# Kernel optimization log

Hardware: AMD Instinct MI355X
Metric: run time of the kernel (lower is better)

The kernel has to match this reference:

```python
import jax, jax.numpy as jnp
import numpy as np

B, S, DM, H = 4, 2048, 768, 12
HD = DM // H
HEAD_Z = float(np.sqrt(HD))


def norm_layer(x, scale, bias):
    # custom normalization over last dim: (x - mean)/std * scale + bias, scalar scale/bias, no eps
    mean = x.mean(axis=2, keepdims=True)
    std = jnp.sqrt(((x - mean) ** 2).mean(axis=2, keepdims=True))
    return (x - mean) / std * scale + bias


def setup_inputs() -> dict:
    key = jax.random.key(0)
    ks = jax.random.split(key, 12)
    s = 1.0 / np.sqrt(DM)
    return {
        "base": jax.random.normal(ks[0], (B, S, DM), dtype=jnp.float32),
        "Wqkv": jax.random.normal(ks[1], (DM, 3 * DM), dtype=jnp.float32) * s,
        "bqkv": jax.random.normal(ks[2], (3 * DM,), dtype=jnp.float32) * s,
        "W1": jax.random.normal(ks[3], (DM, DM), dtype=jnp.float32) * s,
        "b1": jax.random.normal(ks[4], (DM,), dtype=jnp.float32) * s,
        "W2": jax.random.normal(ks[5], (DM, DM), dtype=jnp.float32) * s,
        "b2": jax.random.normal(ks[6], (DM,), dtype=jnp.float32) * s,
        "n1_scale": jax.random.uniform(ks[7], (1,), jnp.float32, -s, s) + 0.5,
        "n1_bias": jax.random.uniform(ks[8], (1,), jnp.float32, -s, s),
        "n2_scale": jax.random.uniform(ks[9], (1,), jnp.float32, -s, s) + 0.5,
        "n2_bias": jax.random.uniform(ks[10], (1,), jnp.float32, -s, s),
    }


def reference(base, Wqkv, bqkv, W1, b1, W2, b2, n1_scale, n1_bias, n2_scale, n2_bias):
    qkv = base @ Wqkv + bqkv                     # [B,S,3*DM]
    q, k, v = jnp.split(qkv, 3, axis=2)
    # per-head attention, vectorized over heads: the torch loop with broadcast-mul-sum
    # is mathematically softmax(QK^T/sqrt(hd)) @ V per head
    q = q.reshape(B, S, H, HD)
    k = k.reshape(B, S, H, HD)
    v = v.reshape(B, S, H, HD)
    scores = jnp.einsum('bqhd,bkhd->bhqk', q, k) / HEAD_Z  # [B,H,S,S]
    attn = jax.nn.softmax(scores, axis=-1)
    av = jnp.einsum('bhqk,bkhd->bqhd', attn, v).reshape(B, S, DM)
    hidden = norm_layer(av @ W1 + b1 + base, n1_scale, n1_bias)
    out = norm_layer(jax.nn.relu(hidden @ W2 + b2) + hidden, n2_scale, n2_bias)
    return out
```

## Files before the change

### kernel.cpp

```cpp
#include <hip/hip_runtime.h>
#include <hip/hip_bf16.h>
#include <stdint.h>

#define B_ 4
#define S_ 2048
#define DM_ 768
#define H_ 12
#define HD_ 64
#define ROWS (B_*S_)
#define QKVN (3*DM_)

typedef __attribute__((ext_vector_type(8))) short short8;
typedef __attribute__((ext_vector_type(4))) float floatx4;
typedef __attribute__((ext_vector_type(8))) unsigned short ushort8;
typedef __attribute__((ext_vector_type(4))) unsigned short ushort4v;
typedef __attribute__((ext_vector_type(4))) float float4_t;

__device__ __forceinline__ unsigned short f2b(float f) {
  union { float f; uint32_t u; } x; x.f = f;
  uint32_t r = x.u + 0x7FFFu + ((x.u >> 16) & 1u);
  return (unsigned short)(r >> 16);
}
__device__ __forceinline__ float b2f(unsigned short u) {
  union { uint32_t u; float f; } x; x.u = ((uint32_t)u) << 16; return x.f;
}
__device__ __forceinline__ uint32_t fbits(float f) {
  union { float f; uint32_t u; } x; x.f = f; return x.u;
}

__device__ __forceinline__ void load_lds16(const void* g, void* l) {
  __builtin_amdgcn_global_load_lds(
      (const __attribute__((address_space(1))) uint32_t*)g,
      (__attribute__((address_space(3))) uint32_t*)l, 16, 0, 0);
}

#define CVT_B 6144
#define WQ_B 1728
#define W1_B 576
__global__ __launch_bounds__(256) void prep(
    const float* __restrict__ base, unsigned short* __restrict__ base_bf,
    const float* __restrict__ Wqkv, unsigned short* __restrict__ Wqkvt,
    const float* __restrict__ W1, unsigned short* __restrict__ W1t,
    const float* __restrict__ W2, unsigned short* __restrict__ W2t) {
  __shared__ float t[32][33];
  int bid = blockIdx.x;
  int tid = threadIdx.x;
  if (bid < CVT_B) {
    int i = bid * 256 + tid;
    float4_t v = ((const float4_t*)base)[i];
    ushort4v o;
    o[0] = f2b(v[0]); o[1] = f2b(v[1]); o[2] = f2b(v[2]); o[3] = f2b(v[3]);
    ((ushort4v*)base_bf)[i] = o;
    return;
  }
  const float* W; unsigned short* Wt; int N, rel;
  if (bid < CVT_B + WQ_B)      { W = Wqkv; Wt = Wqkvt; N = QKVN; rel = bid - CVT_B; }
  else if (bid < CVT_B + WQ_B + W1_B) { W = W1; Wt = W1t; N = DM_; rel = bid - CVT_B - WQ_B; }
  else                          { W = W2; Wt = W2t; N = DM_; rel = bid - CVT_B - WQ_B - W1_B; }
  int K = DM_;
  int n0 = (rel % (N / 32)) * 32, k0 = (rel / (N / 32)) * 32;
  int tx = tid & 31, ty = tid >> 5;
#pragma unroll
  for (int i = 0; i < 4; i++)
    t[ty + i * 8][tx] = W[(size_t)(k0 + ty + i * 8) * N + n0 + tx];
  __syncthreads();
#pragma unroll
  for (int i = 0; i < 4; i++)
    Wt[(size_t)(n0 + ty + i * 8) * K + k0 + tx] = f2b(t[tx][ty + i * 8]);
}

__global__ __launch_bounds__(256) void vtrans(const unsigned short* __restrict__ qkv,
                                              unsigned short* __restrict__ Vt) {
  int st = blockIdx.x;
  int bh = blockIdx.y;
  int b = bh / H_, h = bh % H_;
  __shared__ unsigned short t[64][65];
  int tid = threadIdx.x;
#pragma unroll
  for (int i = 0; i < 2; i++) {
    int c = i * 256 + tid;
    int r = c >> 3, o = (c & 7) * 8;
    ushort8 v = *(const ushort8*)(qkv + (size_t)(b * S_ + st * 64 + r) * QKVN + 2 * DM_ + h * HD_ + o);
#pragma unroll
    for (int j = 0; j < 8; j++) t[r][o + j] = v[j];
  }
  __syncthreads();
#pragma unroll
  for (int i = 0; i < 2; i++) {
    int c = i * 256 + tid;
    int d = c >> 3, o = (c & 7) * 8;
    ushort8 v;
#pragma unroll
    for (int j = 0; j < 8; j++) {
      int p = o + j;
      int s = ((p & 3) << 4) | (p >> 2);
      v[j] = t[s][d];
    }
    *(ushort8*)(Vt + (size_t)(bh * 64 + d) * S_ + st * 64 + o) = v;
  }
}

__global__ __launch_bounds__(256, 2) void gemm_qkv(
    const unsigned short* __restrict__ A,
    const unsigned short* __restrict__ Bt,
    const float* __restrict__ bias,
    unsigned short* __restrict__ Cout,
    int M, int N, int K) {
  __shared__ __align__(16) unsigned short As[128 * 64];
  __shared__ __align__(16) unsigned short Bs[128 * 64];
  int tid = threadIdx.x;
  int wave = tid >> 6, lane = tid & 63;
  int quad = lane >> 4, l16 = lane & 15;
  int e = l16 & 7;
  int sr = lane >> 3;
  int sc = (lane & 7) ^ (sr & 7);
  int m0 = blockIdx.y * 128, n0 = blockIdx.x * 128;
  int wm = (wave >> 1) * 64, wn = (wave & 1) * 64;
  floatx4 acc[4][4] = {};
  int c0 = wave * 4;

  for (int kb = 0; kb < K; kb += 64) {
#pragma unroll
    for (int i = 0; i < 4; i++) {
      int op = c0 + i;
      load_lds16(A + (size_t)(m0 + op * 8 + sr) * K + kb + sc * 8, (char*)As + op * 1024);
    }
#pragma unroll
    for (int i = 0; i < 4; i++) {
      int op = c0 + i;
      load_lds16(Bt + (size_t)(n0 + op * 8 + sr) * K + kb + sc * 8, (char*)Bs + op * 1024);
    }
    __syncthreads();
#pragma unroll
    for (int ks = 0; ks < 2; ks++) {
      short8 af[4], bfr[4];
#pragma unroll
      for (int mt = 0; mt < 4; mt++)
        af[mt] = *(const short8*)(As + (wm + mt * 16 + l16) * 64 + ((ks * 4 + quad) ^ e) * 8);
#pragma unroll
      for (int nt = 0; nt < 4; nt++)
        bfr[nt] = *(const short8*)(Bs + (wn + nt * 16 + l16) * 64 + ((ks * 4 + quad) ^ e) * 8);
#pragma unroll
      for (int mt = 0; mt < 4; mt++)
#pragma unroll
        for (int nt = 0; nt < 4; nt++)
          acc[mt][nt] = __builtin_amdgcn_mfma_f32_16x16x32_bf16(af[mt], bfr[nt], acc[mt][nt], 0, 0, 0);
    }
    __syncthreads();
  }
#pragma unroll
  for (int mt = 0; mt < 4; mt++) {
#pragma unroll
    for (int nt = 0; nt < 4; nt++) {
#pragma unroll
      for (int r = 0; r < 4; r++) {
        int row = m0 + wm + mt * 16 + quad * 4 + r;
        int col = n0 + wn + nt * 16 + l16;
        size_t idx = (size_t)row * N + col;
        float v = acc[mt][nt][r] + bias[col];
        if (col < DM_) v *= 0.18033688011112042f;
        Cout[idx] = f2b(v);
      }
    }
  }
}

template <int EPI>
__global__ __launch_bounds__(256, 4) void gemm64(
    const unsigned short* __restrict__ A,
    const unsigned short* __restrict__ Bt,
    const float* __restrict__ bias,
    const unsigned short* __restrict__ res,
    unsigned short* __restrict__ Cout,
    int M, int N, int K) {
  __shared__ __align__(16) unsigned short As[64 * 64];
  __shared__ __align__(16) unsigned short Bs[128 * 64];
  int tid = threadIdx.x;
  int wave = tid >> 6, lane = tid & 63;
  int quad = lane >> 4, l16 = lane & 15;
  int e = l16 & 7;
  int sr = lane >> 3;
  int sc = (lane & 7) ^ (sr & 7);
  int m0 = blockIdx.y * 64, n0 = blockIdx.x * 128;
  int wm = (wave >> 1) * 32, wn = (wave & 1) * 64;
  floatx4 acc[2][4] = {};

  for (int kb = 0; kb < K; kb += 64) {
#pragma unroll
    for (int i = 0; i < 2; i++) {
      int op = wave * 2 + i;
      load_lds16(A + (size_t)(m0 + op * 8 + sr) * K + kb + sc * 8, (char*)As + op * 1024);
    }
#pragma unroll
    for (int i = 0; i < 4; i++) {
      int op = wave * 4 + i;
      load_lds16(Bt + (size_t)(n0 + op * 8 + sr) * K + kb + sc * 8, (char*)Bs + op * 1024);
    }
    __syncthreads();
#pragma unroll
    for (int ks = 0; ks < 2; ks++) {
      short8 af[2], bfr[4];
#pragma unroll
      for (int mt = 0; mt < 2; mt++)
        af[mt] = *(const short8*)(As + (wm + mt * 16 + l16) * 64 + ((ks * 4 + quad) ^ e) * 8);
#pragma unroll
      for (int nt = 0; nt < 4; nt++)
        bfr[nt] = *(const short8*)(Bs + (wn + nt * 16 + l16) * 64 + ((ks * 4 + quad) ^ e) * 8);
#pragma unroll
      for (int mt = 0; mt < 2; mt++)
#pragma unroll
        for (int nt = 0; nt < 4; nt++)
          acc[mt][nt] = __builtin_amdgcn_mfma_f32_16x16x32_bf16(af[mt], bfr[nt], acc[mt][nt], 0, 0, 0);
    }
    __syncthreads();
  }
#pragma unroll
  for (int mt = 0; mt < 2; mt++) {
#pragma unroll
    for (int nt = 0; nt < 4; nt++) {
#pragma unroll
      for (int r = 0; r < 4; r++) {
        int row = m0 + wm + mt * 16 + quad * 4 + r;
        int col = n0 + wn + nt * 16 + l16;
        size_t idx = (size_t)row * N + col;
        float v = acc[mt][nt][r] + bias[col];
        if (EPI == 2) v = fmaxf(v, 0.0f);
        v += b2f(res[idx]);
        Cout[idx] = f2b(v);
      }
    }
  }
}

__global__ __launch_bounds__(256, 2) void attn(
    const unsigned short* __restrict__ qkv,
    const unsigned short* __restrict__ Vt,
    unsigned short* __restrict__ av) {
  int qt = blockIdx.x;
  int bh = blockIdx.y;
  int b = bh / H_, h = bh % H_;
  int row0 = b * S_ + qt * 128;
  __shared__ __align__(16) unsigned short Ks[2][64 * 64];
  __shared__ __align__(16) unsigned short Vs[2][64 * 64];
  __shared__ __align__(16) unsigned short Ps[4][32 * 72];
  int tid = threadIdx.x;
  int wave = tid >> 6, lane = tid & 63;
  int quad = lane >> 4, l16 = lane & 15;
  int e = l16 & 7;
  int sr = lane >> 3;
  int sc = (lane & 7) ^ (sr & 7);

#pragma unroll
  for (int i = 0; i < 4; i++) {
    load_lds16(qkv + (size_t)(row0 + wave * 32 + i * 8 + sr) * QKVN + h * HD_ + sc * 8,
               (char*)Ps[wave] + i * 1024);
  }
  const unsigned short* kp = qkv + (size_t)(b * S_ + wave * 16 + sr) * QKVN + DM_ + h * HD_ + sc * 8;
  const unsigned short* vp = Vt + ((size_t)bh * 64 + wave * 16 + sr) * S_ + sc * 8;
  auto stageKV = [&](const unsigned short* kq, const unsigned short* vq, int buf) {
#pragma unroll
    for (int i = 0; i < 2; i++) {
      load_lds16(kq + (size_t)i * 8 * QKVN, (char*)Ks[buf] + wave * 2048 + i * 1024);
      load_lds16(vq + (size_t)i * 8 * S_, (char*)Vs[buf] + wave * 2048 + i * 1024);
    }
  };
  stageKV(kp, vp, 0);

  floatx4 accO[2][4] = {};
  floatx4 accL[2] = {};
  short8 ones;
#pragma unroll
  for (int j = 0; j < 8; j++) ones[j] = (short)0x3F80;
  __syncthreads();

  short8 qf[2][2];
#pragma unroll
  for (int mf = 0; mf < 2; mf++)
#pragma unroll
    for (int ks = 0; ks < 2; ks++)
      qf[mf][ks] = *(const short8*)(Ps[wave] + (mf * 16 + l16) * 64 + ((ks * 4 + quad) ^ e) * 8);

  int cur = 0;
  for (int kt = 0; kt < 32; kt++) {
    floatx4 sv[2][4] = {};
#pragma unroll
    for (int ks = 0; ks < 2; ks++)
#pragma unroll
      for (int nt = 0; nt < 4; nt++) {
        short8 kf = *(const short8*)(Ks[cur] + (nt * 16 + l16) * 64 + ((ks * 4 + quad) ^ e) * 8);
#pragma unroll
        for (int mf = 0; mf < 2; mf++)
          sv[mf][nt] = __builtin_amdgcn_mfma_f32_16x16x32_bf16(qf[mf][ks], kf, sv[mf][nt], 0, 0, 0);
      }
    if (kt + 1 < 32) {
      kp += 64 * QKVN;
      vp += 64;
      stageKV(kp, vp, cur ^ 1);
    }
#pragma unroll
    for (int mf = 0; mf < 2; mf++)
#pragma unroll
      for (int r = 0; r < 4; r++) {
        uint32_t u0 = fbits(__builtin_amdgcn_exp2f(sv[mf][0][r]));
        uint32_t u1 = fbits(__builtin_amdgcn_exp2f(sv[mf][1][r]));
        uint32_t u2 = fbits(__builtin_amdgcn_exp2f(sv[mf][2][r]));
        uint32_t u3 = fbits(__builtin_amdgcn_exp2f(sv[mf][3][r]));
        uint2 val;
        val.x = __builtin_amdgcn_perm(u1, u0, 0x07060302u);
        val.y = __builtin_amdgcn_perm(u3, u2, 0x07060302u);
        *(uint2*)(&Ps[wave][(mf * 16 + quad * 4 + r) * 72 + l16 * 4]) = val;
      }
#pragma unroll
    for (int ks = 0; ks < 2; ks++) {
      short8 pf[2];
#pragma unroll
      for (int mf = 0; mf < 2; mf++) {
        pf[mf] = *(const short8*)(Ps[wave] + (mf * 16 + l16) * 72 + ks * 32 + quad * 8);
        accL[mf] = __builtin_amdgcn_mfma_f32_16x16x32_bf16(pf[mf], ones, accL[mf], 0, 0, 0);
      }
#pragma unroll
      for (int nt = 0; nt < 4; nt++) {
        short8 vf = *(const short8*)(Vs[cur] + (nt * 16 + l16) * 64 + ((ks * 4 + quad) ^ e) * 8);
#pragma unroll
        for (int mf = 0; mf < 2; mf++)
          accO[mf][nt] = __builtin_amdgcn_mfma_f32_16x16x32_bf16(pf[mf], vf, accO[mf][nt], 0, 0, 0);
      }
    }
    __syncthreads();
    cur ^= 1;
  }
#pragma unroll
  for (int mf = 0; mf < 2; mf++)
#pragma unroll
    for (int r = 0; r < 4; r++) {
      float inv = 1.0f / accL[mf][r];
      int row = row0 + wave * 32 + mf * 16 + quad * 4 + r;
#pragma unroll
      for (int nt = 0; nt < 4; nt++)
        av[(size_t)row * DM_ + h * HD_ + nt * 16 + l16] = f2b(accO[mf][nt][r] * inv);
    }
}

template <int WB>
__global__ __launch_bounds__(256) void normk(
    const unsigned short* __restrict__ X, const float* __restrict__ scale,
    const float* __restrict__ bias, float* __restrict__ Y,
    unsigned short* __restrict__ Ybf) {
  int row = blockIdx.x;
  const unsigned short* x = X + (size_t)row * DM_;
  int tid = threadIdx.x;
  int wave = tid >> 6, lane = tid & 63;
  float v[3];
#pragma unroll
  for (int i = 0; i < 3; i++) v[i] = b2f(x[tid + i * 256]);
  float s = v[0] + v[1] + v[2];
#pragma unroll
  for (int o = 32; o > 0; o >>= 1) s += __shfl_xor(s, o);
  __shared__ float red[4];
  if (lane == 0) red[wave] = s;
  __syncthreads();
  float mean = (red[0] + red[1] + red[2] + red[3]) * (1.0f / DM_);
  float ss = 0.0f;
#pragma unroll
  for (int i = 0; i < 3; i++) { v[i] -= mean; ss += v[i] * v[i]; }
#pragma unroll
  for (int o = 32; o > 0; o >>= 1) ss += __shfl_xor(ss, o);
  __syncthreads();
  if (lane == 0) red[wave] = ss;
  __syncthreads();
  float var = (red[0] + red[1] + red[2] + red[3]) * (1.0f / DM_);
  float rstd = rsqrtf(var);
  float sg = scale[0], bg = bias[0];
#pragma unroll
  for (int i = 0; i < 3; i++) {
    float y = v[i] * rstd * sg + bg;
    if (WB) Ybf[(size_t)row * DM_ + tid + i * 256] = f2b(y);
    else    Y[(size_t)row * DM_ + tid + i * 256] = y;
  }
}

extern "C" void kernel_launch(void* const* d_in, const int* in_sizes, int n_in,
                              void* d_out, int out_size, void* d_ws, size_t ws_size,
                              hipStream_t stream) {
  const float* base = (const float*)d_in[0];
  const float* Wqkv = (const float*)d_in[1];
  const float* bqkv = (const float*)d_in[2];
  const float* W1 = (const float*)d_in[3];
  const float* b1 = (const float*)d_in[4];
  const float* W2 = (const float*)d_in[5];
  const float* b2 = (const float*)d_in[6];
  const float* n1s = (const float*)d_in[7];
  const float* n1b = (const float*)d_in[8];
  const float* n2s = (const float*)d_in[9];
  const float* n2b = (const float*)d_in[10];
  float* out = (float*)d_out;

  char* ws = (char*)d_ws;
  size_t off = 0;
  auto alloc = [&](size_t bytes) {
    char* p = ws + off;
    off = (off + bytes + 255) & ~(size_t)255;
    return p;
  };
  unsigned short* base_bf = (unsigned short*)alloc((size_t)ROWS * DM_ * 2);
  unsigned short* Wqkvt = (unsigned short*)alloc((size_t)QKVN * DM_ * 2);
  unsigned short* W1t = (unsigned short*)alloc((size_t)DM_ * DM_ * 2);
  unsigned short* W2t = (unsigned short*)alloc((size_t)DM_ * DM_ * 2);
  unsigned short* qkvb = (unsigned short*)alloc((size_t)ROWS * QKVN * 2);
  unsigned short* Vtb = (unsigned short*)alloc((size_t)B_ * H_ * HD_ * S_ * 2);
  unsigned short* avb = (unsigned short*)alloc((size_t)ROWS * DM_ * 2);
  unsigned short* t1b = (unsigned short*)alloc((size_t)ROWS * DM_ * 2);
  unsigned short* hbf = (unsigned short*)alloc((size_t)ROWS * DM_ * 2);

  prep<<<CVT_B + WQ_B + 2 * W1_B, 256, 0, stream>>>(
      base, base_bf, Wqkv, Wqkvt, W1, W1t, W2, W2t);
  gemm_qkv<<<dim3(QKVN / 128, ROWS / 128), 256, 0, stream>>>(
      base_bf, Wqkvt, bqkv, qkvb, ROWS, QKVN, DM_);
  vtrans<<<dim3(S_ / 64, B_ * H_), 256, 0, stream>>>(qkvb, Vtb);
  attn<<<dim3(S_ / 128, B_ * H_), 256, 0, stream>>>(qkvb, Vtb, avb);
  gemm64<1><<<dim3(DM_ / 128, ROWS / 64), 256, 0, stream>>>(
      avb, W1t, b1, base_bf, t1b, ROWS, DM_, DM_);
  normk<1><<<ROWS, 256, 0, stream>>>(t1b, n1s, n1b, nullptr, hbf);
  gemm64<2><<<dim3(DM_ / 128, ROWS / 64), 256, 0, stream>>>(
      hbf, W2t, b2, hbf, t1b, ROWS, DM_, DM_);
  normk<0><<<ROWS, 256, 0, stream>>>(t1b, n2s, n2b, out, nullptr);
}
```

Before: 258.2 us.

## Fuse V transpose into QKV GEMM epilogue and widen K tile to 128

Removes the separate vtrans kernel. The QKV GEMM now writes the V block directly in transposed per-head layout, staging through LDS in the epilogue, and writes Q and K normally. The K-step is doubled to 128 with a 16-way XOR swizzle, which halves the number of barriers per tile. In exchange, LDS use rises to 64KB per block, which may reduce occupancy below the launch bound's target of 2 blocks. The transposed layout must match what attn expects, since the old vtrans applied a permuted s ordering.

```diff
diff --git a/kernel.cpp b/kernel.cpp
--- a/kernel.cpp
+++ b/kernel.cpp
@@ -69,77 +69,50 @@
     Wt[(size_t)(n0 + ty + i * 8) * K + k0 + tx] = f2b(t[tx][ty + i * 8]);
 }
 
-__global__ __launch_bounds__(256) void vtrans(const unsigned short* __restrict__ qkv,
-                                              unsigned short* __restrict__ Vt) {
-  int st = blockIdx.x;
-  int bh = blockIdx.y;
-  int b = bh / H_, h = bh % H_;
-  __shared__ unsigned short t[64][65];
-  int tid = threadIdx.x;
-#pragma unroll
-  for (int i = 0; i < 2; i++) {
-    int c = i * 256 + tid;
-    int r = c >> 3, o = (c & 7) * 8;
-    ushort8 v = *(const ushort8*)(qkv + (size_t)(b * S_ + st * 64 + r) * QKVN + 2 * DM_ + h * HD_ + o);
-#pragma unroll
-    for (int j = 0; j < 8; j++) t[r][o + j] = v[j];
-  }
-  __syncthreads();
-#pragma unroll
-  for (int i = 0; i < 2; i++) {
-    int c = i * 256 + tid;
-    int d = c >> 3, o = (c & 7) * 8;
-    ushort8 v;
-#pragma unroll
-    for (int j = 0; j < 8; j++) {
-      int p = o + j;
-      int s = ((p & 3) << 4) | (p >> 2);
-      v[j] = t[s][d];
-    }
-    *(ushort8*)(Vt + (size_t)(bh * 64 + d) * S_ + st * 64 + o) = v;
-  }
-}
-
 __global__ __launch_bounds__(256, 2) void gemm_qkv(
     const unsigned short* __restrict__ A,
     const unsigned short* __restrict__ Bt,
     const float* __restrict__ bias,
     unsigned short* __restrict__ Cout,
+    unsigned short* __restrict__ Vt,
     int M, int N, int K) {
-  __shared__ __align__(16) unsigned short As[128 * 64];
-  __shared__ __align__(16) unsigned short Bs[128 * 64];
+  __shared__ __align__(16) unsigned short LDSbuf[2 * 128 * 128];
+  unsigned short* As = LDSbuf;
+  unsigned short* Bs = LDSbuf + 128 * 128;
   int tid = threadIdx.x;
   int wave = tid >> 6, lane = tid & 63;
   int quad = lane >> 4, l16 = lane & 15;
-  int e = l16 & 7;
-  int sr = lane >> 3;
-  int sc = (lane & 7) ^ (sr & 7);
+  int sr4 = lane >> 4;
+  int c16 = lane & 15;
   int m0 = blockIdx.y * 128, n0 = blockIdx.x * 128;
   int wm = (wave >> 1) * 64, wn = (wave & 1) * 64;
   floatx4 acc[4][4] = {};
-  int c0 = wave * 4;
-
-  for (int kb = 0; kb < K; kb += 64) {
-#pragma unroll
-    for (int i = 0; i < 4; i++) {
-      int op = c0 + i;
-      load_lds16(A + (size_t)(m0 + op * 8 + sr) * K + kb + sc * 8, (char*)As + op * 1024);
-    }
-#pragma unroll
-    for (int i = 0; i < 4; i++) {
-      int op = c0 + i;
-      load_lds16(Bt + (size_t)(n0 + op * 8 + sr) * K + kb + sc * 8, (char*)Bs + op * 1024);
+
+  for (int kb = 0; kb < K; kb += 128) {
+#pragma unroll
+    for (int i = 0; i < 8; i++) {
+      int op = wave * 8 + i;
+      int srow = op * 4 + sr4;
+      int sc = c16 ^ (srow & 15);
+      load_lds16(A + (size_t)(m0 + srow) * K + kb + sc * 8, (char*)As + op * 1024);
+    }
+#pragma unroll
+    for (int i = 0; i < 8; i++) {
+      int op = wave * 8 + i;
+      int srow = op * 4 + sr4;
+      int sc = c16 ^ (srow & 15);
+      load_lds16(Bt + (size_t)(n0 + srow) * K + kb + sc * 8, (char*)Bs + op * 1024);
     }
     __syncthreads();
 #pragma unroll
-    for (int ks = 0; ks < 2; ks++) {
+    for (int ks = 0; ks < 4; ks++) {
       short8 af[4], bfr[4];
 #pragma unroll
       for (int mt = 0; mt < 4; mt++)
-        af[mt] = *(const short8*)(As + (wm + mt * 16 + l16) * 64 + ((ks * 4 + quad) ^ e) * 8);
+        af[mt] = *(const short8*)(As + (wm + mt * 16 + l16) * 128 + ((ks * 4 + quad) ^ l16) * 8);
 #pragma unroll
       for (int nt = 0; nt < 4; nt++)
-        bfr[nt] = *(const short8*)(Bs + (wn + nt * 16 + l16) * 64 + ((ks * 4 + quad) ^ e) * 8);
+        bfr[nt] = *(const short8*)(Bs + (wn + nt * 16 + l16) * 128 + ((ks * 4 + quad) ^ l16) * 8);
 #pragma unroll
       for (int mt = 0; mt < 4; mt++)
 #pragma unroll
@@ -148,19 +121,45 @@
     }
     __syncthreads();
   }
-#pragma unroll
-  for (int mt = 0; mt < 4; mt++) {
+
+  if (n0 < 2 * DM_) {
+#pragma unroll
+    for (int mt = 0; mt < 4; mt++) {
+#pragma unroll
+      for (int nt = 0; nt < 4; nt++) {
+#pragma unroll
+        for (int r = 0; r < 4; r++) {
+          int row = m0 + wm + mt * 16 + quad * 4 + r;
+          int col = n0 + wn + nt * 16 + l16;
+          float v = acc[mt][nt][r] + bias[col];
+          if (col < DM_) v *= 0.18033688011112042f;
+          Cout[(size_t)row * N + col] = f2b(v);
+        }
+      }
+    }
+  } else {
+    unsigned short* scr = LDSbuf + wave * 4608;
+    int h = (n0 + wn - 2 * DM_) >> 6;
+    int b = m0 >> 11;
+    int s_base = (m0 & (S_ - 1)) + wm;
 #pragma unroll
     for (int nt = 0; nt < 4; nt++) {
-#pragma unroll
-      for (int r = 0; r < 4; r++) {
-        int row = m0 + wm + mt * 16 + quad * 4 + r;
-        int col = n0 + wn + nt * 16 + l16;
-        size_t idx = (size_t)row * N + col;
-        float v = acc[mt][nt][r] + bias[col];
-        if (col < DM_) v *= 0.18033688011112042f;
-        Cout[idx] = f2b(v);
-      }
+      float bv = bias[n0 + wn + nt * 16 + l16];
+      ushort8 v0, v1;
+#pragma unroll
+      for (int j = 0; j < 8; j++) {
+        v0[j] = f2b(acc[j & 3][nt][j >> 2] + bv);
+        v1[j] = f2b(acc[j & 3][nt][2 + (j >> 2)] + bv);
+      }
+      *(ushort8*)(scr + (nt * 16 + l16) * 72 + quad * 16) = v0;
+      *(ushort8*)(scr + (nt * 16 + l16) * 72 + quad * 16 + 8) = v1;
+    }
+#pragma unroll
+    for (int it = 0; it < 8; it++) {
+      int d = it * 8 + (lane >> 3);
+      int ch = lane & 7;
+      ushort8 w = *(const ushort8*)(scr + d * 72 + ch * 8);
+      *(ushort8*)(Vt + ((size_t)(b * H_ + h) * 64 + d) * S_ + s_base + ch * 8) = w;
     }
   }
 }
@@ -415,8 +414,7 @@
   prep<<<CVT_B + WQ_B + 2 * W1_B, 256, 0, stream>>>(
       base, base_bf, Wqkv, Wqkvt, W1, W1t, W2, W2t);
   gemm_qkv<<<dim3(QKVN / 128, ROWS / 128), 256, 0, stream>>>(
-      base_bf, Wqkvt, bqkv, qkvb, ROWS, QKVN, DM_);
-  vtrans<<<dim3(S_ / 64, B_ * H_), 256, 0, stream>>>(qkvb, Vtb);
+      base_bf, Wqkvt, bqkv, qkvb, Vtb, ROWS, QKVN, DM_);
   attn<<<dim3(S_ / 128, B_ * H_), 256, 0, stream>>>(qkvb, Vtb, avb);
   gemm64<1><<<dim3(DM_ / 128, ROWS / 64), 256, 0, stream>>>(
       avb, W1t, b1, base_bf, t1b, ROWS, DM_, DM_);
```

New measurement: 254.7 us. No clear change (-1.3%).
